# Kernel tuning notes

Measured on AMD Instinct MI355X. Metric: run time of the kernel, lower is better.

The kernel has to match this reference:

```python
import jax, jax.numpy as jnp
import numpy as np

B, T, H = 32, 2000, 512      # batch, encoder frames, d_model
L = 256                      # max label length (padded output tokens)
THRESHOLD = 0.95


def setup_inputs() -> dict:
    key = jax.random.key(0)
    k1, k2, k3 = jax.random.split(key, 3)
    hidden = jax.random.normal(k1, (B, T, H), dtype=jnp.float32)
    alphas = jax.random.uniform(k2, (B, T), dtype=jnp.float32)
    target_lengths = jax.random.randint(k3, (B,), 64, L + 1)
    return {"hidden": hidden, "alphas": alphas, "target_lengths": target_lengths}


def _cif(hidden, alphas):
    # Continuous integrate-and-fire scan over time.
    Bt, Tt, Ht = hidden.shape

    def step(carry, xs):
        integrate, frame = carry          # [B], [B,H]
        alpha, h = xs                     # [B], [B,H]
        dist_completion = 1.0 - integrate
        integrate = integrate + alpha
        fire = integrate >= THRESHOLD     # [B] bool
        cur = jnp.where(fire, dist_completion, alpha)
        remainds = alpha - cur
        frame_out = frame + cur[:, None] * h
        integ_next = jnp.where(fire, integrate - 1.0, integrate)
        frame_next = jnp.where(fire[:, None], remainds[:, None] * h, frame_out)
        return (integ_next, frame_next), (frame_out, fire)

    init = (jnp.zeros((Bt,), hidden.dtype), jnp.zeros((Bt, Ht), hidden.dtype))
    _, (frames, fires) = jax.lax.scan(step, init, (alphas.T, jnp.swapaxes(hidden, 0, 1)))
    frames = jnp.swapaxes(frames, 0, 1)   # [B,T,H] accumulated frame at each step
    fires = fires.T                        # [B,T] fire events

    # Gather fired frames into padded [B, L, H] token tensor (vectorized scatter).
    tok = jnp.cumsum(fires.astype(jnp.int32), axis=1) - 1   # token index per fired frame
    valid = fires & (tok >= 0) & (tok < L)
    out = jnp.zeros((Bt, L, Ht), hidden.dtype)
    b_idx = jnp.arange(Bt)[:, None]
    out = out.at[b_idx, jnp.clip(tok, 0, L - 1)].add(
        frames * valid[..., None].astype(hidden.dtype))
    return out


def reference(hidden, alphas, target_lengths):
    # Rescale alphas so each row sums to target length (noise term omitted).
    num = target_lengths.astype(alphas.dtype)
    alphas = alphas * (num / alphas.sum(-1))[:, None]
    return _cif(hidden, alphas)
```

## Files before the change

### kernel.cpp

```cpp
#include <hip/hip_runtime.h>

#define BB 32
#define TT 2000
#define NG 500
#define HH 512
#define LL 256
#define THRESH 0.95f

#define CHUNK 512
#define NCH 4
#define BPB 8
#define SPAD 9
#define NWIN 16


__global__ __launch_bounds__(256) void cif_scale_kernel(
    const float* __restrict__ alphas, const int* __restrict__ tlen,
    float* __restrict__ scale_g)
{
    const int b = blockIdx.x;
    const int tid = threadIdx.x;
    __shared__ double red[256];
    const float4* a4 = (const float4*)(alphas + b * TT);
    double s = 0.0;
    for (int g = tid; g < NG; g += 256) {
        float4 v = a4[g];
        s += (double)v.x + (double)v.y + (double)v.z + (double)v.w;
    }
    red[tid] = s;
    __syncthreads();
    for (int off = 128; off > 0; off >>= 1) {
        if (tid < off) red[tid] += red[tid + off];
        __syncthreads();
    }
    if (tid == 0)
        scale_g[b] = (float)tlen[b] / (float)red[0];
}

__global__ __launch_bounds__(256) void cif_scan_kernel(
    const float* __restrict__ alphas, const float* __restrict__ scale_g,
    int2* __restrict__ rec, int* __restrict__ nfires)
{
    const int b0 = blockIdx.x * BPB;
    const int tid = threadIdx.x;
    __shared__ float saT[CHUNK * SPAD];
    __shared__ float ipT[CHUNK * SPAD];
    __shared__ unsigned smask[NWIN * BPB];
    __shared__ float scs[BPB];

    if (tid < BPB) scs[tid] = scale_g[b0 + tid];
    __syncthreads();

    float integ = 0.0f;
    float carry_in = 0.0f;
    int tok = 0;

    for (int c = 0; c < NCH; ++c) {
        {
            const int bl = tid >> 5;
            const int lane = tid & 31;
            const float sc = scs[bl];
            const float* arow = alphas + (size_t)(b0 + bl) * TT + c * CHUNK;
            #pragma unroll
            for (int j = 0; j < CHUNK / 32; ++j) {
                const int t = lane + j * 32;
                const int gt = c * CHUNK + t;
                const float a = (gt < TT) ? arow[t] : 0.0f;
                saT[t * SPAD + bl] = a * sc;
            }
        }
        __syncthreads();

        if (tid < BPB) {
            carry_in = integ;
            for (int w = 0; w < NWIN; ++w) {
                unsigned mask = 0;
                #pragma unroll
                for (int j = 0; j < 32; ++j) {
                    const int t = w * 32 + j;
                    const float a = saT[t * SPAD + tid];
                    float ii = integ + a;
                    const bool fire = (ii >= THRESH);
                    const float iim1 = ii - 1.0f;
                    ii = fire ? iim1 : ii;
                    mask |= fire ? (1u << j) : 0u;
                    ipT[t * SPAD + tid] = ii;
                    integ = ii;
                }
                smask[w * BPB + tid] = mask;
            }
        }
        __syncthreads();

        if (tid < BPB) {
            const int b = b0 + tid;
            for (int w = 0; w < NWIN; ++w) {
                unsigned m = smask[w * BPB + tid];
                while (m) {
                    const int j = __ffs(m) - 1;
                    m &= m - 1;
                    const int t = w * 32 + j;
                    if (tok < LL) {
                        const float prev = (t == 0) ? carry_in
                                                    : ipT[(t - 1) * SPAD + tid];
                        int2 r;
                        r.x = c * CHUNK + t;
                        r.y = __float_as_int(1.0f - prev);
                        rec[b * LL + tok] = r;
                    }
                    ++tok;
                }
            }
        }
        __syncthreads();
    }
    if (tid < BPB) nfires[b0 + tid] = (tok < LL) ? tok : LL;
}

__global__ __launch_bounds__(128) void cif_gather_kernel(
    const float* __restrict__ hidden, const float* __restrict__ alphas,
    const float* __restrict__ scale_g, const int2* __restrict__ rec,
    const int* __restrict__ nfires, float* __restrict__ out)
{
    const int l = blockIdx.x;
    const int b = blockIdx.y;
    const int tid = threadIdx.x;

    float4 acc = make_float4(0.f, 0.f, 0.f, 0.f);
    const int F = nfires[b];
    if (l < F) {
        const int2 re = rec[b * LL + l];
        const int e = re.x;
        const float dist = __int_as_float(re.y);
        const float sc = scale_g[b];
        const float* hb = hidden + (size_t)b * TT * HH + (size_t)tid * 4;
        const float* ab = alphas + b * TT;
        int t0 = 0;
        if (l > 0) {
            const int2 rp = rec[b * LL + l - 1];
            const int sp = rp.x;
            const float dp = __int_as_float(rp.y);
            const float rem = ab[sp] * sc - dp;
            const float4 hv = *(const float4*)(hb + (size_t)sp * HH);
            acc.x = rem * hv.x; acc.y = rem * hv.y;
            acc.z = rem * hv.z; acc.w = rem * hv.w;
            t0 = sp + 1;
        }
        int t = t0;
        float w0 = (t < e) ? ab[t] * sc : dist;
        float4 h0 = *(const float4*)(hb + (size_t)t * HH);
        if (t < e) {
            float w1 = (t + 1 < e) ? ab[t + 1] * sc : dist;
            float4 h1 = *(const float4*)(hb + (size_t)(t + 1) * HH);
            while (t + 2 <= e) {
                const float w2 = (t + 2 < e) ? ab[t + 2] * sc : dist;
                const float4 h2 = *(const float4*)(hb + (size_t)(t + 2) * HH);
                acc.x += w0 * h0.x; acc.y += w0 * h0.y;
                acc.z += w0 * h0.z; acc.w += w0 * h0.w;
                w0 = w1; h0 = h1; w1 = w2; h1 = h2; ++t;
            }
            acc.x += w0 * h0.x; acc.y += w0 * h0.y;
            acc.z += w0 * h0.z; acc.w += w0 * h0.w;
            w0 = w1; h0 = h1;
        }
        acc.x += w0 * h0.x; acc.y += w0 * h0.y;
        acc.z += w0 * h0.z; acc.w += w0 * h0.w;
    }
    *(float4*)(out + ((size_t)b * LL + l) * HH + (size_t)tid * 4) = acc;
}

extern "C" void kernel_launch(void* const* d_in, const int* in_sizes, int n_in,
                              void* d_out, int out_size, void* d_ws, size_t ws_size,
                              hipStream_t stream) {
    const float* hidden = (const float*)d_in[0];
    const float* alphas = (const float*)d_in[1];
    const int*   tlen   = (const int*)d_in[2];
    float* out = (float*)d_out;

    int2*  rec     = (int2*)d_ws;
    int*   nfires  = (int*)(rec + BB * LL);
    float* scale_g = (float*)(nfires + BB);

    cif_scale_kernel<<<BB, 256, 0, stream>>>(alphas, tlen, scale_g);
    cif_scan_kernel<<<4, 256, 0, stream>>>(alphas, scale_g, rec, nfires);
    cif_gather_kernel<<<dim3(LL, BB), 128, 0, stream>>>(hidden, alphas, scale_g,
                                                        rec, nfires, out);
}
```

Baseline: 284.9 us.

## Stage whole alpha rows in LDS and fuse fire detection into single scan

The scan kernel now loads each batch row's full scaled alphas into shared memory at once with float4 loads, instead of four chunked transposed passes. A single serial loop per row prefetches float4 registers, detects fires and writes fire records directly into a shared list, with no separate mask-decode pass and no per-chunk barriers. The list is then copied to global memory cooperatively by all threads. Shared memory use grows to roughly 80KB per block, and the serial thread now reads strided float4 rows, which may raise LDS bank conflicts.

```diff
diff --git a/kernel.cpp b/kernel.cpp
--- a/kernel.cpp
+++ b/kernel.cpp
@@ -7,11 +7,8 @@
 #define LL 256
 #define THRESH 0.95f
 
-#define CHUNK 512
-#define NCH 4
 #define BPB 8
-#define SPAD 9
-#define NWIN 16
+#define RSTRIDE 2004
 
 
 __global__ __launch_bounds__(256) void cif_scale_kernel(
@@ -43,78 +40,84 @@
 {
     const int b0 = blockIdx.x * BPB;
     const int tid = threadIdx.x;
-    __shared__ float saT[CHUNK * SPAD];
-    __shared__ float ipT[CHUNK * SPAD];
-    __shared__ unsigned smask[NWIN * BPB];
+    __shared__ float sa[BPB * RSTRIDE];
+    __shared__ int2 flist[BPB * LL];
     __shared__ float scs[BPB];
 
     if (tid < BPB) scs[tid] = scale_g[b0 + tid];
     __syncthreads();
 
-    float integ = 0.0f;
-    float carry_in = 0.0f;
-    int tok = 0;
+    {
+        const int r = tid >> 5;
+        const int lane = tid & 31;
+        const float sc = scs[r];
+        const float4* arow4 = (const float4*)(alphas + (size_t)(b0 + r) * TT);
+        float4* srow4 = (float4*)(sa + r * RSTRIDE);
+        #pragma unroll
+        for (int j = 0; j < NG / 32; ++j) {
+            const int g = lane + j * 32;
+            float4 v = arow4[g];
+            v.x *= sc; v.y *= sc; v.z *= sc; v.w *= sc;
+            srow4[g] = v;
+        }
+        const int g = lane + (NG / 32) * 32;
+        if (g < NG) {
+            float4 v = arow4[g];
+            v.x *= sc; v.y *= sc; v.z *= sc; v.w *= sc;
+            srow4[g] = v;
+        }
+    }
+    __syncthreads();
 
-    for (int c = 0; c < NCH; ++c) {
-        {
-            const int bl = tid >> 5;
-            const int lane = tid & 31;
-            const float sc = scs[bl];
-            const float* arow = alphas + (size_t)(b0 + bl) * TT + c * CHUNK;
+    int nf = 0;
+    if (tid < BPB) {
+        const float4* s4 = (const float4*)(sa + tid * RSTRIDE);
+        int2* fl = flist + tid * LL;
+        float integ = 0.0f;
+
+        float4 rbuf[4];
+        #pragma unroll
+        for (int i = 0; i < 4; ++i) rbuf[i] = s4[i];
+
+        for (int blk = 0; blk < 125; ++blk) {
             #pragma unroll
-            for (int j = 0; j < CHUNK / 32; ++j) {
-                const int t = lane + j * 32;
-                const int gt = c * CHUNK + t;
-                const float a = (gt < TT) ? arow[t] : 0.0f;
-                saT[t * SPAD + bl] = a * sc;
-            }
-        }
-        __syncthreads();
-
-        if (tid < BPB) {
-            carry_in = integ;
-            for (int w = 0; w < NWIN; ++w) {
-                unsigned mask = 0;
+            for (int i = 0; i < 4; ++i) {
+                const int g = blk * 4 + i;
+                const float4 c = rbuf[i];
+                if (g + 4 < NG) rbuf[i] = s4[g + 4];
+                const float av[4] = {c.x, c.y, c.z, c.w};
                 #pragma unroll
-                for (int j = 0; j < 32; ++j) {
-                    const int t = w * 32 + j;
-                    const float a = saT[t * SPAD + tid];
+                for (int j = 0; j < 4; ++j) {
+                    const float a = av[j];
+                    const float dist = 1.0f - integ;
                     float ii = integ + a;
                     const bool fire = (ii >= THRESH);
                     const float iim1 = ii - 1.0f;
                     ii = fire ? iim1 : ii;
-                    mask |= fire ? (1u << j) : 0u;
-                    ipT[t * SPAD + tid] = ii;
+                    if (fire) {
+                        if (nf < LL) {
+                            int2 r;
+                            r.x = g * 4 + j;
+                            r.y = __float_as_int(dist);
+                            fl[nf] = r;
+                        }
+                        ++nf;
+                    }
                     integ = ii;
-                }
-                smask[w * BPB + tid] = mask;
-            }
-        }
-        __syncthreads();
-
-        if (tid < BPB) {
-            const int b = b0 + tid;
-            for (int w = 0; w < NWIN; ++w) {
-                unsigned m = smask[w * BPB + tid];
-                while (m) {
-                    const int j = __ffs(m) - 1;
-                    m &= m - 1;
-                    const int t = w * 32 + j;
-                    if (tok < LL) {
-                        const float prev = (t == 0) ? carry_in
-                                                    : ipT[(t - 1) * SPAD + tid];
-                        int2 r;
-                        r.x = c * CHUNK + t;
-                        r.y = __float_as_int(1.0f - prev);
-                        rec[b * LL + tok] = r;
-                    }
-                    ++tok;
                 }
             }
         }
-        __syncthreads();
     }
-    if (tid < BPB) nfires[b0 + tid] = (tok < LL) ? tok : LL;
+    __syncthreads();
+
+    {
+        int2* rg = rec + b0 * LL;
+        const int2* fs = flist;
+        #pragma unroll
+        for (int j = 0; j < (BPB * LL) / 256; ++j)
+            rg[tid + j * 256] = fs[tid + j * 256];
+    }
+    if (tid < BPB) nfires[b0 + tid] = (nf < LL) ? nf : LL;
 }
 
 __global__ __launch_bounds__(128) void cif_gather_kernel(
```

New measurement: 304.0 us. 1.07x slower.

## Pre-transpose scaled alphas and parallelize fire-record emission across windows

Applied to the files above, without the earlier changes.

The scale kernel now also writes a time-major, pre-scaled copy of alphas to workspace. The scan then runs as a single block in which 32 threads each scan one batch row, reading from global memory with register prefetch and saving a fire mask plus the end-of-window integrator per 32-step window. A prefix sum over per-window fire counts lets all 256 threads re-scan their windows in parallel and write the fire records, replacing the serial per-fire emission pass and the shared-memory chunk staging. The trade-off is that the serial scan now depends on global load latency in a single block, plus an extra workspace write and the re-scan work.

```diff
diff --git a/kernel.cpp b/kernel.cpp
--- a/kernel.cpp
+++ b/kernel.cpp
@@ -2,25 +2,22 @@
 
 #define BB 32
 #define TT 2000
+#define TP 2048
+#define NWIN 63
 #define NG 500
 #define HH 512
 #define LL 256
 #define THRESH 0.95f
 
-#define CHUNK 512
-#define NCH 4
-#define BPB 8
-#define SPAD 9
-#define NWIN 16
-
 
 __global__ __launch_bounds__(256) void cif_scale_kernel(
     const float* __restrict__ alphas, const int* __restrict__ tlen,
-    float* __restrict__ scale_g)
+    float* __restrict__ scale_g, float* __restrict__ alphasT)
 {
     const int b = blockIdx.x;
     const int tid = threadIdx.x;
     __shared__ double red[256];
+    __shared__ float s_sc;
     const float4* a4 = (const float4*)(alphas + b * TT);
     double s = 0.0;
     for (int g = tid; g < NG; g += 256) {
@@ -33,88 +30,91 @@
         if (tid < off) red[tid] += red[tid + off];
         __syncthreads();
     }
-    if (tid == 0)
-        scale_g[b] = (float)tlen[b] / (float)red[0];
+    if (tid == 0) {
+        const float sc = (float)tlen[b] / (float)red[0];
+        scale_g[b] = sc;
+        s_sc = sc;
+    }
+    __syncthreads();
+    const float sc = s_sc;
+    for (int t = tid; t < TP; t += 256)
+        alphasT[t * BB + b] = (t < TT) ? alphas[b * TT + t] * sc : 0.0f;
 }
 
 __global__ __launch_bounds__(256) void cif_scan_kernel(
-    const float* __restrict__ alphas, const float* __restrict__ scale_g,
-    int2* __restrict__ rec, int* __restrict__ nfires)
+    const float* __restrict__ alphasT, int2* __restrict__ rec,
+    int* __restrict__ nfires)
 {
-    const int b0 = blockIdx.x * BPB;
     const int tid = threadIdx.x;
-    __shared__ float saT[CHUNK * SPAD];
-    __shared__ float ipT[CHUNK * SPAD];
-    __shared__ unsigned smask[NWIN * BPB];
-    __shared__ float scs[BPB];
+    __shared__ unsigned smask[NWIN * BB];
+    __shared__ float sinteg[NWIN * BB];
+    __shared__ int spre[NWIN * BB];
 
-    if (tid < BPB) scs[tid] = scale_g[b0 + tid];
+    if (tid < BB) {
+        const float* colp = alphasT + tid;
+        float rb[32];
+        #pragma unroll
+        for (int j = 0; j < 32; ++j) rb[j] = colp[j * BB];
+        float integ = 0.0f;
+        for (int w = 0; w < NWIN; ++w) {
+            const float* nxt = colp + (size_t)(w + 1) * 32 * BB;
+            unsigned mask = 0;
+            #pragma unroll
+            for (int j = 0; j < 32; ++j) {
+                const float a = rb[j];
+                rb[j] = nxt[j * BB];
+                float ii = integ + a;
+                const bool fire = (ii >= THRESH);
+                const float iim1 = ii - 1.0f;
+                ii = fire ? iim1 : ii;
+                mask |= fire ? (1u << j) : 0u;
+                integ = ii;
+            }
+            smask[w * BB + tid] = mask;
+            sinteg[w * BB + tid] = integ;
+        }
+    }
     __syncthreads();
 
-    float integ = 0.0f;
-    float carry_in = 0.0f;
-    int tok = 0;
+    if (tid < BB) {
+        int run = 0;
+        for (int w = 0; w < NWIN; ++w) {
+            spre[w * BB + tid] = run;
+            run += __popc(smask[w * BB + tid]);
+        }
+        nfires[tid] = (run < LL) ? run : LL;
+    }
+    __syncthreads();
 
-    for (int c = 0; c < NCH; ++c) {
-        {
-            const int bl = tid >> 5;
-            const int lane = tid & 31;
-            const float sc = scs[bl];
-            const float* arow = alphas + (size_t)(b0 + bl) * TT + c * CHUNK;
-            #pragma unroll
-            for (int j = 0; j < CHUNK / 32; ++j) {
-                const int t = lane + j * 32;
-                const int gt = c * CHUNK + t;
-                const float a = (gt < TT) ? arow[t] : 0.0f;
-                saT[t * SPAD + bl] = a * sc;
-            }
-        }
-        __syncthreads();
-
-        if (tid < BPB) {
-            carry_in = integ;
-            for (int w = 0; w < NWIN; ++w) {
-                unsigned mask = 0;
-                #pragma unroll
+    for (int r = 0; r < 8; ++r) {
+        const int tau = tid + r * 256;
+        if (tau < NWIN * BB) {
+            const int w = tau >> 5;
+            const int b = tau & 31;
+            const unsigned m = smask[w * BB + b];
+            if (m) {
+                float integ = (w == 0) ? 0.0f : sinteg[(w - 1) * BB + b];
+                int tok = spre[w * BB + b];
+                const float* col = alphasT + b;
                 for (int j = 0; j < 32; ++j) {
-                    const int t = w * 32 + j;
-                    const float a = saT[t * SPAD + tid];
+                    const float a = col[(size_t)(w * 32 + j) * BB];
+                    const float dist = 1.0f - integ;
                     float ii = integ + a;
-                    const bool fire = (ii >= THRESH);
-                    const float iim1 = ii - 1.0f;
-                    ii = fire ? iim1 : ii;
-                    mask |= fire ? (1u << j) : 0u;
-                    ipT[t * SPAD + tid] = ii;
+                    if (ii >= THRESH) {
+                        if (tok < LL) {
+                            int2 rr;
+                            rr.x = w * 32 + j;
+                            rr.y = __float_as_int(dist);
+                            rec[b * LL + tok] = rr;
+                        }
+                        ++tok;
+                        ii -= 1.0f;
+                    }
                     integ = ii;
-                }
-                smask[w * BPB + tid] = mask;
-            }
-        }
-        __syncthreads();
-
-        if (tid < BPB) {
-            const int b = b0 + tid;
-            for (int w = 0; w < NWIN; ++w) {
-                unsigned m = smask[w * BPB + tid];
-                while (m) {
-                    const int j = __ffs(m) - 1;
-                    m &= m - 1;
-                    const int t = w * 32 + j;
-                    if (tok < LL) {
-                        const float prev = (t == 0) ? carry_in
-                                                    : ipT[(t - 1) * SPAD + tid];
-                        int2 r;
-                        r.x = c * CHUNK + t;
-                        r.y = __float_as_int(1.0f - prev);
-                        rec[b * LL + tok] = r;
-                    }
-                    ++tok;
                 }
             }
         }
-        __syncthreads();
     }
-    if (tid < BPB) nfires[b0 + tid] = (tok < LL) ? tok : LL;
 }
 
 __global__ __launch_bounds__(128) void cif_gather_kernel(
@@ -177,12 +177,13 @@
     const int*   tlen   = (const int*)d_in[2];
     float* out = (float*)d_out;
 
-    int2*  rec     = (int2*)d_ws;
+    float* alphasT = (float*)d_ws;
+    int2*  rec     = (int2*)(alphasT + TP * BB);
     int*   nfires  = (int*)(rec + BB * LL);
     float* scale_g = (float*)(nfires + BB);
 
-    cif_scale_kernel<<<BB, 256, 0, stream>>>(alphas, tlen, scale_g);
-    cif_scan_kernel<<<4, 256, 0, stream>>>(alphas, scale_g, rec, nfires);
+    cif_scale_kernel<<<BB, 256, 0, stream>>>(alphas, tlen, scale_g, alphasT);
+    cif_scan_kernel<<<1, 256, 0, stream>>>(alphasT, rec, nfires);
     cif_gather_kernel<<<dim3(LL, BB), 128, 0, stream>>>(hidden, alphas, scale_g,
                                                         rec, nfires, out);
 }
```

Result: slower. 297.4 us (+4.4%).
